# Kernel optimization log

Hardware: AMD Instinct MI355X
Metric: run time of the kernel (lower is better)

Reference implementation:

```python
import jax, jax.numpy as jnp
import numpy as np

B = 4096
N = 4097  # num_samples; basis fit uses N-1 columns


def _trapz_cumsum(x, t):
    # y[..., 0] = 0; y[..., i] = y[..., i-1] + 0.5*(t[i]-t[i-1])*(x[..., i-1]+x[..., i])
    dt = t[1:] - t[:-1]                                   # (N-1,)
    inc = 0.5 * dt * (x[..., :-1] + x[..., 1:])           # (B,1,N-1)
    zero = jnp.zeros(x.shape[:-1] + (1,), x.dtype)
    return jnp.concatenate([zero, jnp.cumsum(inc, axis=-1)], axis=-1)  # (B,1,N)


def setup_inputs() -> dict:
    key = jax.random.key(0)
    k1, k2 = jax.random.split(key)
    # positive signal so ny + cumsum(x) stays > 0 (needed for pow/log)
    x = jax.random.uniform(k1, (B, 1, N), dtype=jnp.float32, minval=0.1, maxval=1.1)
    # strictly increasing time grid
    dt = jax.random.uniform(k2, (N,), dtype=jnp.float32, minval=1e-3, maxval=1e-2)
    t = jnp.cumsum(dt)
    params = jnp.array([0.5, 1.0], dtype=jnp.float32)  # [r, ny]
    return {"x": x, "t": t, "params": params}


def reference(x, t, params):
    r, ny = params[0], params[1]
    y = _trapz_cumsum(x, t)                  # (B,1,N)
    z = ny + y[:, 0, 1:]                     # (B,N-1)
    phi = jnp.stack([z, z ** r], axis=1)     # (B,2,N-1)  basis matrix
    phip = jnp.linalg.pinv(phi)              # (B,N-1,2)
    x_sl = x[:, :, 1:]                       # (B,1,N-1)
    coeffs = x_sl @ phip                     # (B,1,2)
    x_hat = coeffs @ phi                     # (B,1,N-1)
    res = x_sl - x_hat                       # (B,1,N-1)
    r2 = jnp.sum(res ** 2, axis=-1)          # (B,1)
    return coeffs, x_hat, res, r2
```

## Files before the change

### kernel.cpp

```cpp
#include <hip/hip_runtime.h>

constexpr int NPTS = 4097;
constexpr int M    = 4096;
constexpr int TPB  = 256;
constexpr int NJ   = 4;

__global__ __launch_bounds__(TPB)
void vp_kernel(const float* __restrict__ x, const float* __restrict__ t,
               const float* __restrict__ params, float* __restrict__ out, int B)
{
    const int b    = blockIdx.x;
    const int tid  = threadIdx.x;
    const int lane = tid & 63;
    const int wid  = tid >> 6;

    const float r  = params[0];
    const float ny = params[1];

    const float* __restrict__ xrow = x + (size_t)b * NPTS;

    float xs[NJ][4];
    float zl[NJ][4];
    float gs[NJ];

#pragma unroll
    for (int j = 0; j < NJ; ++j) {
        const int e = j * 1024 + tid * 4;
        float x0 = xrow[e],     x1 = xrow[e + 1], x2 = xrow[e + 2];
        float x3 = xrow[e + 3], x4 = xrow[e + 4];
        float4 tq = *reinterpret_cast<const float4*>(t + e);
        float  tn = t[e + 4];
        float i0 = 0.5f * (tq.y - tq.x) * (x0 + x1);
        float i1 = 0.5f * (tq.z - tq.y) * (x1 + x2);
        float i2 = 0.5f * (tq.w - tq.z) * (x2 + x3);
        float i3 = 0.5f * (tn   - tq.w) * (x3 + x4);
        zl[j][0] = i0;
        zl[j][1] = i0 + i1;
        zl[j][2] = i0 + i1 + i2;
        zl[j][3] = i0 + i1 + i2 + i3;
        gs[j] = zl[j][3];
        xs[j][0] = x1; xs[j][1] = x2; xs[j][2] = x3; xs[j][3] = x4;
    }

    float sc0 = gs[0], sc1 = gs[1], sc2 = gs[2], sc3 = gs[3];
#pragma unroll
    for (int d = 1; d < 64; d <<= 1) {
        float u0 = __shfl_up(sc0, d, 64);
        float u1 = __shfl_up(sc1, d, 64);
        float u2 = __shfl_up(sc2, d, 64);
        float u3 = __shfl_up(sc3, d, 64);
        if (lane >= d) { sc0 += u0; sc1 += u1; sc2 += u2; sc3 += u3; }
    }

    __shared__ float  wt[TPB / 64][NJ];
    __shared__ double wred[TPB / 64][6];
    __shared__ float  cbc[2];

    if (lane == 63) {
        wt[wid][0] = sc0; wt[wid][1] = sc1; wt[wid][2] = sc2; wt[wid][3] = sc3;
    }
    __syncthreads();

    float woff[NJ] = {0, 0, 0, 0};
    float Tj[NJ]   = {0, 0, 0, 0};
#pragma unroll
    for (int w = 0; w < TPB / 64; ++w) {
#pragma unroll
        for (int j = 0; j < NJ; ++j) {
            float v = wt[w][j];
            Tj[j] += v;
            if (w < wid) woff[j] += v;
        }
    }
    float zbase[NJ];
    float jacc = 0.f;
    float scv[NJ] = {sc0, sc1, sc2, sc3};
#pragma unroll
    for (int j = 0; j < NJ; ++j) {
        zbase[j] = ny + jacc + woff[j] + (scv[j] - gs[j]);
        jacc += Tj[j];
    }

    double szz = 0, szw = 0, sww = 0, sxz = 0, sxw = 0;
#pragma unroll
    for (int j = 0; j < NJ; ++j) {
#pragma unroll
        for (int i = 0; i < 4; ++i) {
            float z = zbase[j] + zl[j][i];
            zl[j][i] = z;
            float w = (r == 0.5f) ? sqrtf(z) : powf(z, r);
            float xv = xs[j][i];
            szz += (double)z  * (double)z;
            szw += (double)z  * (double)w;
            sww += (double)w  * (double)w;
            sxz += (double)xv * (double)z;
            sxw += (double)xv * (double)w;
        }
    }
#pragma unroll
    for (int d = 32; d > 0; d >>= 1) {
        szz += __shfl_down(szz, d, 64);
        szw += __shfl_down(szw, d, 64);
        sww += __shfl_down(sww, d, 64);
        sxz += __shfl_down(sxz, d, 64);
        sxw += __shfl_down(sxw, d, 64);
    }
    if (lane == 0) {
        wred[wid][0] = szz; wred[wid][1] = szw; wred[wid][2] = sww;
        wred[wid][3] = sxz; wred[wid][4] = sxw;
    }
    __syncthreads();

    if (tid == 0) {
        double a0 = 0, a1 = 0, a2 = 0, a3 = 0, a4 = 0;
        for (int w = 0; w < TPB / 64; ++w) {
            a0 += wred[w][0]; a1 += wred[w][1]; a2 += wred[w][2];
            a3 += wred[w][3]; a4 += wred[w][4];
        }
        double det = a0 * a2 - a1 * a1;
        double inv = 1.0 / det;
        double c0 = (a3 * a2 - a4 * a1) * inv;
        double c1 = (a4 * a0 - a3 * a1) * inv;
        out[(size_t)b * 2 + 0] = (float)c0;
        out[(size_t)b * 2 + 1] = (float)c1;
        cbc[0] = (float)c0; cbc[1] = (float)c1;
    }
    __syncthreads();
    const float c0 = cbc[0], c1 = cbc[1];

    float* __restrict__ xhat = out + (size_t)B * 2 + (size_t)b * M;
    float* __restrict__ res  = xhat + (size_t)B * M;

    double r2 = 0;
#pragma unroll
    for (int j = 0; j < NJ; ++j) {
        const int e = j * 1024 + tid * 4;
        float h[4], ev[4];
#pragma unroll
        for (int i = 0; i < 4; ++i) {
            float z = zl[j][i];
            float w = (r == 0.5f) ? sqrtf(z) : powf(z, r);
            h[i]  = c0 * z + c1 * w;
            ev[i] = xs[j][i] - h[i];
            r2 += (double)ev[i] * (double)ev[i];
        }
        *reinterpret_cast<float4*>(xhat + e) = make_float4(h[0], h[1], h[2], h[3]);
        *reinterpret_cast<float4*>(res  + e) = make_float4(ev[0], ev[1], ev[2], ev[3]);
    }
#pragma unroll
    for (int d = 32; d > 0; d >>= 1) r2 += __shfl_down(r2, d, 64);
    if (lane == 0) wred[wid][5] = r2;
    __syncthreads();
    if (tid == 0) {
        double s = 0;
        for (int w = 0; w < TPB / 64; ++w) s += wred[w][5];
        out[(size_t)B * 2 + 2 * (size_t)B * M + b] = (float)s;
    }
}

extern "C" void kernel_launch(void* const* d_in, const int* in_sizes, int n_in,
                              void* d_out, int out_size, void* d_ws, size_t ws_size,
                              hipStream_t stream) {
    const float* x = (const float*)d_in[0];
    const float* t = (const float*)d_in[1];
    const float* p = (const float*)d_in[2];
    float* out     = (float*)d_out;
    const int B    = in_sizes[0] / NPTS;

    vp_kernel<<<dim3(B), dim3(TPB), 0, stream>>>(x, t, p, out, B);
}
```

Baseline: 42.61 us.

## Use aligned vector loads, shuffle time neighbors, redundant solve, nontemporal stores

The x row starts at a misaligned offset (row stride 4097). Each row is now specialised by its offset (b&3) so it can use two aligned 16-byte loads instead of five scalar loads per thread. The t[e+4] load is replaced by a wave shuffle, with only lane 63 going to memory. Every thread now redundantly computes the 2x2 solve, which removes one __syncthreads and the shared broadcast. Output stores become nontemporal. The costs are extra over-read, more code through the four template variants, and possible register pressure.

```diff
diff --git a/kernel.cpp b/kernel.cpp
--- a/kernel.cpp
+++ b/kernel.cpp
@@ -1,9 +1,45 @@
 #include <hip/hip_runtime.h>
+
+typedef float f32x4 __attribute__((ext_vector_type(4)));
 
 constexpr int NPTS = 4097;
 constexpr int M    = 4096;
 constexpr int TPB  = 256;
+constexpr int NW   = TPB / 64;
 constexpr int NJ   = 4;
+
+template<int S>
+__device__ __forceinline__ void load_scan(
+    const float* __restrict__ xrow, const float* __restrict__ t,
+    int tid, int lane,
+    float (&xs)[NJ][4], float (&zl)[NJ][4], float (&gs)[NJ])
+{
+    const float* __restrict__ xal = xrow - S;
+#pragma unroll
+    for (int j = 0; j < NJ; ++j) {
+        const int e = j * 1024 + tid * 4;
+        const f32x4 a4 = *reinterpret_cast<const f32x4*>(xal + e);
+        const f32x4 c4 = *reinterpret_cast<const f32x4*>(xal + e + 4);
+        const float cmb[8] = {a4.x, a4.y, a4.z, a4.w, c4.x, c4.y, c4.z, c4.w};
+        const float x0 = cmb[S + 0], x1 = cmb[S + 1], x2 = cmb[S + 2],
+                    x3 = cmb[S + 3], x4 = cmb[S + 4];
+
+        const f32x4 tq = *reinterpret_cast<const f32x4*>(t + e);
+        float tn = __shfl_down(tq.x, 1, 64);
+        if (lane == 63) tn = t[e + 4];
+
+        const float i0 = 0.5f * (tq.y - tq.x) * (x0 + x1);
+        const float i1 = 0.5f * (tq.z - tq.y) * (x1 + x2);
+        const float i2 = 0.5f * (tq.w - tq.z) * (x2 + x3);
+        const float i3 = 0.5f * (tn   - tq.w) * (x3 + x4);
+        zl[j][0] = i0;
+        zl[j][1] = i0 + i1;
+        zl[j][2] = i0 + i1 + i2;
+        zl[j][3] = i0 + i1 + i2 + i3;
+        gs[j] = zl[j][3];
+        xs[j][0] = x1; xs[j][1] = x2; xs[j][2] = x3; xs[j][3] = x4;
+    }
+}
 
 __global__ __launch_bounds__(TPB)
 void vp_kernel(const float* __restrict__ x, const float* __restrict__ t,
@@ -19,27 +55,18 @@
 
     const float* __restrict__ xrow = x + (size_t)b * NPTS;
 
+    __shared__ float  wt[NW][NJ];
+    __shared__ double wred[NW][6];
+
     float xs[NJ][4];
     float zl[NJ][4];
     float gs[NJ];
 
-#pragma unroll
-    for (int j = 0; j < NJ; ++j) {
-        const int e = j * 1024 + tid * 4;
-        float x0 = xrow[e],     x1 = xrow[e + 1], x2 = xrow[e + 2];
-        float x3 = xrow[e + 3], x4 = xrow[e + 4];
-        float4 tq = *reinterpret_cast<const float4*>(t + e);
-        float  tn = t[e + 4];
-        float i0 = 0.5f * (tq.y - tq.x) * (x0 + x1);
-        float i1 = 0.5f * (tq.z - tq.y) * (x1 + x2);
-        float i2 = 0.5f * (tq.w - tq.z) * (x2 + x3);
-        float i3 = 0.5f * (tn   - tq.w) * (x3 + x4);
-        zl[j][0] = i0;
-        zl[j][1] = i0 + i1;
-        zl[j][2] = i0 + i1 + i2;
-        zl[j][3] = i0 + i1 + i2 + i3;
-        gs[j] = zl[j][3];
-        xs[j][0] = x1; xs[j][1] = x2; xs[j][2] = x3; xs[j][3] = x4;
+    switch (b & 3) {
+    case 0: load_scan<0>(xrow, t, tid, lane, xs, zl, gs); break;
+    case 1: load_scan<1>(xrow, t, tid, lane, xs, zl, gs); break;
+    case 2: load_scan<2>(xrow, t, tid, lane, xs, zl, gs); break;
+    default: load_scan<3>(xrow, t, tid, lane, xs, zl, gs); break;
     }
 
     float sc0 = gs[0], sc1 = gs[1], sc2 = gs[2], sc3 = gs[3];
@@ -52,10 +79,6 @@
         if (lane >= d) { sc0 += u0; sc1 += u1; sc2 += u2; sc3 += u3; }
     }
 
-    __shared__ float  wt[TPB / 64][NJ];
-    __shared__ double wred[TPB / 64][6];
-    __shared__ float  cbc[2];
-
     if (lane == 63) {
         wt[wid][0] = sc0; wt[wid][1] = sc1; wt[wid][2] = sc2; wt[wid][3] = sc3;
     }
@@ -64,7 +87,7 @@
     float woff[NJ] = {0, 0, 0, 0};
     float Tj[NJ]   = {0, 0, 0, 0};
 #pragma unroll
-    for (int w = 0; w < TPB / 64; ++w) {
+    for (int w = 0; w < NW; ++w) {
 #pragma unroll
         for (int j = 0; j < NJ; ++j) {
             float v = wt[w][j];
@@ -74,7 +97,7 @@
     }
     float zbase[NJ];
     float jacc = 0.f;
-    float scv[NJ] = {sc0, sc1, sc2, sc3};
+    const float scv[NJ] = {sc0, sc1, sc2, sc3};
 #pragma unroll
     for (int j = 0; j < NJ; ++j) {
         zbase[j] = ny + jacc + woff[j] + (scv[j] - gs[j]);
@@ -111,50 +134,53 @@
     }
     __syncthreads();
 
-    if (tid == 0) {
-        double a0 = 0, a1 = 0, a2 = 0, a3 = 0, a4 = 0;
-        for (int w = 0; w < TPB / 64; ++w) {
-            a0 += wred[w][0]; a1 += wred[w][1]; a2 += wred[w][2];
-            a3 += wred[w][3]; a4 += wred[w][4];
-        }
+    double a0 = 0, a1 = 0, a2 = 0, a3 = 0, a4 = 0;
+#pragma unroll
+    for (int w = 0; w < NW; ++w) {
+        a0 += wred[w][0]; a1 += wred[w][1]; a2 += wred[w][2];
+        a3 += wred[w][3]; a4 += wred[w][4];
+    }
+    {
         double det = a0 * a2 - a1 * a1;
         double inv = 1.0 / det;
-        double c0 = (a3 * a2 - a4 * a1) * inv;
-        double c1 = (a4 * a0 - a3 * a1) * inv;
-        out[(size_t)b * 2 + 0] = (float)c0;
-        out[(size_t)b * 2 + 1] = (float)c1;
-        cbc[0] = (float)c0; cbc[1] = (float)c1;
-    }
-    __syncthreads();
-    const float c0 = cbc[0], c1 = cbc[1];
+        double c0d = (a3 * a2 - a4 * a1) * inv;
+        double c1d = (a4 * a0 - a3 * a1) * inv;
+        if (tid == 0) {
+            out[(size_t)b * 2 + 0] = (float)c0d;
+            out[(size_t)b * 2 + 1] = (float)c1d;
+        }
+        const float c0 = (float)c0d, c1 = (float)c1d;
 
-    float* __restrict__ xhat = out + (size_t)B * 2 + (size_t)b * M;
-    float* __restrict__ res  = xhat + (size_t)B * M;
+        float* __restrict__ xhat = out + (size_t)B * 2 + (size_t)b * M;
+        float* __restrict__ res  = xhat + (size_t)B * M;
 
-    double r2 = 0;
+        double r2 = 0;
 #pragma unroll
-    for (int j = 0; j < NJ; ++j) {
-        const int e = j * 1024 + tid * 4;
-        float h[4], ev[4];
+        for (int j = 0; j < NJ; ++j) {
+            const int e = j * 1024 + tid * 4;
+            float h[4], ev[4];
 #pragma unroll
-        for (int i = 0; i < 4; ++i) {
-            float z = zl[j][i];
-            float w = (r == 0.5f) ? sqrtf(z) : powf(z, r);
-            h[i]  = c0 * z + c1 * w;
-            ev[i] = xs[j][i] - h[i];
-            r2 += (double)ev[i] * (double)ev[i];
+            for (int i = 0; i < 4; ++i) {
+                float z = zl[j][i];
+                float w = (r == 0.5f) ? sqrtf(z) : powf(z, r);
+                h[i]  = c0 * z + c1 * w;
+                ev[i] = xs[j][i] - h[i];
+                r2 += (double)ev[i] * (double)ev[i];
+            }
+            f32x4 hv = {h[0], h[1], h[2], h[3]};
+            f32x4 rv = {ev[0], ev[1], ev[2], ev[3]};
+            __builtin_nontemporal_store(hv, reinterpret_cast<f32x4*>(xhat + e));
+            __builtin_nontemporal_store(rv, reinterpret_cast<f32x4*>(res + e));
         }
-        *reinterpret_cast<float4*>(xhat + e) = make_float4(h[0], h[1], h[2], h[3]);
-        *reinterpret_cast<float4*>(res  + e) = make_float4(ev[0], ev[1], ev[2], ev[3]);
-    }
 #pragma unroll
-    for (int d = 32; d > 0; d >>= 1) r2 += __shfl_down(r2, d, 64);
-    if (lane == 0) wred[wid][5] = r2;
-    __syncthreads();
-    if (tid == 0) {
-        double s = 0;
-        for (int w = 0; w < TPB / 64; ++w) s += wred[w][5];
-        out[(size_t)B * 2 + 2 * (size_t)B * M + b] = (float)s;
+        for (int d = 32; d > 0; d >>= 1) r2 += __shfl_down(r2, d, 64);
+        if (lane == 0) wred[wid][5] = r2;
+        __syncthreads();
+        if (tid == 0) {
+            double s = 0;
+            for (int w = 0; w < NW; ++w) s += wred[w][5];
+            out[(size_t)B * 2 + 2 * (size_t)B * M + b] = (float)s;
+        }
     }
 }
 
```

Measured after the change: 49.88 us. 17.1% more time.
